# Kernel optimization log

Measured on AMD Instinct MI355X. Metric: run time of the kernel, lower is better.

## Reference

```python
import jax, jax.numpy as jnp
import numpy as np

D = 768
H = 12
W = 128
HD = D // H
EPS = 1e-5


def setup_inputs() -> dict:
    key = jax.random.key(0)
    ks = jax.random.split(key, 10)
    B, L = 4, 8190
    s = 1.0 / np.sqrt(D)
    inp = {
        "expanded": jax.random.normal(ks[0], (B, L, D), dtype=jnp.float32),
        "Wq": jax.random.normal(ks[1], (D, D), dtype=jnp.float32) * s,
        "bq": jnp.zeros((D,), jnp.float32),
        "Wk": jax.random.normal(ks[2], (D, D), dtype=jnp.float32) * s,
        "bk": jnp.zeros((D,), jnp.float32),
        "Wv": jax.random.normal(ks[3], (D, D), dtype=jnp.float32) * s,
        "bv": jnp.zeros((D,), jnp.float32),
        "Wo": jax.random.normal(ks[4], (D, D), dtype=jnp.float32) * s,
        "bo": jnp.zeros((D,), jnp.float32),
        "ln_g": jnp.ones((D,), jnp.float32),
        "ln_b": jnp.zeros((D,), jnp.float32),
    }
    return inp


def _local_attn(x, Wq, bq, Wk, bk, Wv, bv, Wo, bo):
    # x: (B, Lp, D) with Lp % W == 0; block-local multihead attention per window
    B, Lp, _ = x.shape
    nW = Lp // W
    xw = x.reshape(B, nW, W, D)
    q = (xw @ Wq + bq).reshape(B, nW, W, H, HD)
    k = (xw @ Wk + bk).reshape(B, nW, W, H, HD)
    v = (xw @ Wv + bv).reshape(B, nW, W, H, HD)
    scale = 1.0 / jnp.sqrt(jnp.asarray(HD, x.dtype))
    # scores: (B, nW, H, W, W)
    scores = jnp.einsum("bnqhd,bnkhd->bnhqk", q, k) * scale
    p = jax.nn.softmax(scores, axis=-1)
    o = jnp.einsum("bnhqk,bnkhd->bnqhd", p, v).reshape(B, nW, W, D)
    o = o @ Wo + bo
    return o.reshape(B, Lp, D)


def reference(expanded, Wq, bq, Wk, bk, Wv, bv, Wo, bo, ln_g, ln_b):
    B, L, _ = expanded.shape
    pad_len = (W - L % W) % W
    x = jnp.pad(expanded, ((0, 0), (0, pad_len), (0, 0))) if pad_len > 0 else expanded
    attn = _local_attn(x, Wq, bq, Wk, bk, Wv, bv, Wo, bo)
    attn = attn[:, :L, :]
    y = expanded + attn
    mu = jnp.mean(y, axis=-1, keepdims=True)
    var = jnp.mean(jnp.square(y - mu), axis=-1, keepdims=True)
    return (y - mu) * jax.lax.rsqrt(var + EPS) * ln_g + ln_b
```

## Files before the change

### kernel.cpp

```cpp
#include <hip/hip_runtime.h>
#include <hip/hip_bf16.h>

#define D 768
#define NQKV 2304
#define NH 12
#define HD 64
#define BATCH 4
#define LSEQ 8190
#define LPAD 8192
#define TP (BATCH*LPAD)

typedef __bf16 bf16x8 __attribute__((ext_vector_type(8)));
typedef float f32x4 __attribute__((ext_vector_type(4)));
using bf16 = __hip_bfloat16;

__device__ __forceinline__ float b2f(bf16 x){ return __bfloat162float(x); }
__device__ __forceinline__ bf16 f2b(float x){ return __float2bfloat16(x); }
__device__ __forceinline__ f32x4 mfma16(bf16x8 a, bf16x8 b, f32x4 c){
    return __builtin_amdgcn_mfma_f32_16x16x32_bf16(a, b, c, 0, 0, 0);
}
__device__ __forceinline__ void gload_lds16(const void* g, void* l){
    __builtin_amdgcn_global_load_lds(
        (const __attribute__((address_space(1))) unsigned int*)g,
        (__attribute__((address_space(3))) unsigned int*)l, 16, 0, 0);
}

__global__ void k_transpose(const float* __restrict__ w0, const float* __restrict__ w1,
                            const float* __restrict__ w2, const float* __restrict__ w3,
                            bf16* __restrict__ WqkvT, bf16* __restrict__ WoT) {
    const float* src; bf16* dst;
    switch (blockIdx.y) {
        case 0:  src = w0; dst = WqkvT;               break;
        case 1:  src = w1; dst = WqkvT + D * D;       break;
        case 2:  src = w2; dst = WqkvT + 2 * D * D;   break;
        default: src = w3; dst = WoT;                 break;
    }
    int o = blockIdx.x * 256 + threadIdx.x;
    int n = o / D, k = o % D;
    dst[o] = f2b(src[k * D + n]);
}

__global__ __launch_bounds__(256) void k_prep(const float* __restrict__ X,
                                              bf16* __restrict__ Xb, int tok0)
{
    int idx = (blockIdx.x * 256 + threadIdx.x) * 8;
    int row = idx / D, col = idx % D;
    int gt = tok0 + row, b = gt >> 13, pos = gt & 8191;
    bf16 tmp[8];
    if (pos < LSEQ) {
        const float* s = &X[((size_t)b * LSEQ + pos) * D + col];
        float4 f0 = *reinterpret_cast<const float4*>(s);
        float4 f1 = *reinterpret_cast<const float4*>(s + 4);
        tmp[0]=f2b(f0.x); tmp[1]=f2b(f0.y); tmp[2]=f2b(f0.z); tmp[3]=f2b(f0.w);
        tmp[4]=f2b(f1.x); tmp[5]=f2b(f1.y); tmp[6]=f2b(f1.z); tmp[7]=f2b(f1.w);
    } else {
        #pragma unroll
        for (int j = 0; j < 8; ++j) tmp[j] = f2b(0.f);
    }
    *reinterpret_cast<uint4*>(&Xb[idx]) = *reinterpret_cast<const uint4*>(tmp);
}

__global__ __launch_bounds__(512, 2) void k_gemm_qkv(
    const bf16* __restrict__ Xb, const bf16* __restrict__ Wt,
    const float* __restrict__ bq, const float* __restrict__ bk, const float* __restrict__ bv,
    bf16* __restrict__ Qkv)
{
    __shared__ alignas(16) bf16 a_lds[4 * 8192];
    __shared__ alignas(16) bf16 b_lds[4 * 8192];

    const int tid = threadIdx.x;
    const int wave = tid >> 6, lane = tid & 63, quad = lane >> 4, lm = lane & 15;
    const int wm = wave >> 2, wn = wave & 3;

    int bid = blockIdx.x;
    const int nwg = gridDim.x;
    if ((nwg & 7) == 0) { const int cpx = nwg >> 3; bid = (bid & 7) * cpx + (bid >> 3); }
    const int rt = bid / 9, ct = bid % 9;

    const int r_loc = tid >> 2;
    const int swslot = ((tid & 3) ^ ((r_loc >> 1) & 3)) * 8;
    const bf16* a_src = Xb + (size_t)(rt * 256 + r_loc) * D + swslot;
    const bf16* b_src = Wt + (size_t)(ct * 256 + r_loc) * D + swslot;
    const int dA = wave * 512;

    #pragma unroll
    for (int pt = 0; pt < 3; ++pt) {
        bf16* ab = a_lds + pt * 8192;
        bf16* bb = b_lds + pt * 8192;
        const int ko = pt * 32;
        gload_lds16(a_src + ko,           ab + dA);
        gload_lds16(a_src + 128 * D + ko, ab + 4096 + dA);
        gload_lds16(b_src + ko,           bb + dA);
        gload_lds16(b_src + 128 * D + ko, bb + 4096 + dA);
    }
    asm volatile("s_waitcnt vmcnt(8)" ::: "memory");
    __builtin_amdgcn_s_barrier();

    const int sw = (quad ^ ((lm >> 1) & 3)) * 8;
    const int aoff = (wm * 128 + lm) * 32 + sw;
    const int boff = (wn * 64 + lm) * 32 + sw;

    f32x4 acc[8][4] = {};

    #pragma unroll 1
    for (int t = 0; t < 24; ++t) {
        const bf16* ab = a_lds + (t & 3) * 8192;
        const bf16* bb = b_lds + (t & 3) * 8192;

        bf16x8 af[4], bfr[4];
        #pragma unroll
        for (int i = 0; i < 4; ++i)
            af[i] = *reinterpret_cast<const bf16x8*>(&ab[aoff + i * 512]);
        #pragma unroll
        for (int n = 0; n < 4; ++n)
            bfr[n] = *reinterpret_cast<const bf16x8*>(&bb[boff + n * 512]);
        if (t < 21) {
            bf16* abn = a_lds + ((t + 3) & 3) * 8192;
            const int ko = (t + 3) * 32;
            gload_lds16(a_src + ko,           abn + dA);
            gload_lds16(a_src + 128 * D + ko, abn + 4096 + dA);
        }
        __builtin_amdgcn_s_barrier();
        __builtin_amdgcn_s_setprio(1);
        #pragma unroll
        for (int i = 0; i < 4; ++i)
            #pragma unroll
            for (int n = 0; n < 4; ++n)
                acc[i][n] = mfma16(af[i], bfr[n], acc[i][n]);
        __builtin_amdgcn_s_setprio(0);
        __builtin_amdgcn_s_barrier();

        bf16x8 ag[4];
        #pragma unroll
        for (int i = 0; i < 4; ++i)
            ag[i] = *reinterpret_cast<const bf16x8*>(&ab[aoff + (i + 4) * 512]);
        if (t < 21) {
            bf16* bbn = b_lds + ((t + 3) & 3) * 8192;
            const int ko = (t + 3) * 32;
            gload_lds16(b_src + ko,           bbn + dA);
            gload_lds16(b_src + 128 * D + ko, bbn + 4096 + dA);
        }
        __builtin_amdgcn_s_barrier();
        __builtin_amdgcn_s_setprio(1);
        #pragma unroll
        for (int i = 0; i < 4; ++i)
            #pragma unroll
            for (int n = 0; n < 4; ++n)
                acc[i + 4][n] = mfma16(ag[i], bfr[n], acc[i + 4][n]);
        __builtin_amdgcn_s_setprio(0);

        if (t <= 20)      asm volatile("s_waitcnt vmcnt(8)" ::: "memory");
        else if (t == 21) asm volatile("s_waitcnt vmcnt(4)" ::: "memory");
        else if (t == 22) asm volatile("s_waitcnt vmcnt(0)" ::: "memory");
        if (t < 23) __builtin_amdgcn_s_barrier();
    }

    const float* bias; int cb;
    if (ct < 3)      { bias = bq; cb = ct * 256; }
    else if (ct < 6) { bias = bk; cb = ct * 256 - D; }
    else             { bias = bv; cb = ct * 256 - 2 * D; }
    float bvv[4];
    #pragma unroll
    for (int n = 0; n < 4; ++n)
        bvv[n] = bias[cb + wn * 64 + n * 16 + lm];

    const int row0 = rt * 256 + wm * 128 + quad * 4;
    const int col0 = ct * 256 + wn * 64 + lm;
    #pragma unroll
    for (int i = 0; i < 8; ++i)
        #pragma unroll
        for (int reg = 0; reg < 4; ++reg) {
            size_t r = (size_t)(row0 + i * 16 + reg) * NQKV;
            #pragma unroll
            for (int n = 0; n < 4; ++n)
                Qkv[r + col0 + n * 16] = f2b(acc[i][n][reg] + bvv[n]);
        }
}

__global__ __launch_bounds__(256) void k_oproj(
    const bf16* __restrict__ Aq, const bf16* __restrict__ WoT,
    const float* __restrict__ bo, const float* __restrict__ X,
    float* __restrict__ out, int tok0)
{
    __shared__ bf16 a_lds[128 * 32];
    __shared__ bf16 b_lds[128 * 32];
    const int tid = threadIdx.x;
    const int rt = blockIdx.x, ct = blockIdx.y;
    const int wave = tid >> 6, lane = tid & 63, quad = lane >> 4, lm = lane & 15;
    const int wm = wave >> 1, wn = wave & 1;
    const int seg0 = wave * 2, seg1 = seg0 + 1;
    const int srow = lane >> 2, selem = (lane & 3) * 8;

    const bf16* Ag = Aq + (size_t)(rt * 128) * NQKV;
    const bf16* Bg = WoT + (size_t)(ct * 128) * D;

    f32x4 acc[4][4] = {};

    for (int kt = 0; kt < D; kt += 32) {
        gload_lds16(Ag + (size_t)(seg0 * 16 + srow) * NQKV + kt + selem, &a_lds[seg0 * 512]);
        gload_lds16(Ag + (size_t)(seg1 * 16 + srow) * NQKV + kt + selem, &a_lds[seg1 * 512]);
        gload_lds16(Bg + (size_t)(seg0 * 16 + srow) * D + kt + selem, &b_lds[seg0 * 512]);
        gload_lds16(Bg + (size_t)(seg1 * 16 + srow) * D + kt + selem, &b_lds[seg1 * 512]);
        __syncthreads();
        bf16x8 af[4], bfr[4];
        #pragma unroll
        for (int i = 0; i < 4; ++i)
            af[i] = *reinterpret_cast<const bf16x8*>(&a_lds[(wm * 64 + i * 16 + lm) * 32 + quad * 8]);
        #pragma unroll
        for (int n = 0; n < 4; ++n)
            bfr[n] = *reinterpret_cast<const bf16x8*>(&b_lds[(wn * 64 + n * 16 + lm) * 32 + quad * 8]);
        #pragma unroll
        for (int i = 0; i < 4; ++i)
            #pragma unroll
            for (int n = 0; n < 4; ++n)
                acc[i][n] = mfma16(af[i], bfr[n], acc[i][n]);
        __syncthreads();
    }

    float bvv[4];
    #pragma unroll
    for (int n = 0; n < 4; ++n)
        bvv[n] = bo[ct * 128 + wn * 64 + n * 16 + lm];

    #pragma unroll
    for (int i = 0; i < 4; ++i)
        #pragma unroll
        for (int reg = 0; reg < 4; ++reg) {
            int g = tok0 + rt * 128 + wm * 64 + i * 16 + quad * 4 + reg;
            int b = g >> 13, pos = g & 8191;
            if (pos >= LSEQ) continue;
            size_t orow = (size_t)b * LSEQ + pos;
            #pragma unroll
            for (int n = 0; n < 4; ++n) {
                int col = ct * 128 + wn * 64 + n * 16 + lm;
                out[orow * D + col] = acc[i][n][reg] + bvv[n] + X[orow * D + col];
            }
        }
}

__global__ __launch_bounds__(256) void k_attn(bf16* Qkv)
{
    __shared__ bf16 qk_lds[2 * 128 * 72];
    __shared__ bf16 vt_lds[64 * 136];
    const int tid = threadIdx.x;
    const int g0 = blockIdx.x * 128, hc = blockIdx.y * 64;
    const int wave = tid >> 6, lane = tid & 63, quad = lane >> 4, lm = lane & 15;
    const int wq = wave * 32;
    bf16* Q_lds = qk_lds;
    bf16* K_lds = qk_lds + 128 * 72;
    bf16* P_lds = qk_lds;

    #pragma unroll
    for (int p = 0; p < 4; ++p) {
        int cid = tid + p * 256;
        int r = cid >> 3, cc = (cid & 7) * 8;
        size_t rb = (size_t)(g0 + r) * NQKV;
        *reinterpret_cast<uint4*>(&Q_lds[r * 72 + cc]) =
            *reinterpret_cast<const uint4*>(&Qkv[rb + hc + cc]);
        *reinterpret_cast<uint4*>(&K_lds[r * 72 + cc]) =
            *reinterpret_cast<const uint4*>(&Qkv[rb + D + hc + cc]);
        uint4 vv = *reinterpret_cast<const uint4*>(&Qkv[rb + 2 * D + hc + cc]);
        const bf16* ve = reinterpret_cast<const bf16*>(&vv);
        #pragma unroll
        for (int j = 0; j < 8; ++j) vt_lds[(cc + j) * 136 + r] = ve[j];
    }
    __syncthreads();

    f32x4 s[2][8] = {};
    #pragma unroll
    for (int ks = 0; ks < HD; ks += 32) {
        bf16x8 aq[2];
        #pragma unroll
        for (int i = 0; i < 2; ++i)
            aq[i] = *reinterpret_cast<const bf16x8*>(&Q_lds[(wq + i * 16 + lm) * 72 + ks + quad * 8]);
        #pragma unroll
        for (int nt = 0; nt < 8; ++nt) {
            bf16x8 bk = *reinterpret_cast<const bf16x8*>(&K_lds[(nt * 16 + lm) * 72 + ks + quad * 8]);
            s[0][nt] = mfma16(aq[0], bk, s[0][nt]);
            s[1][nt] = mfma16(aq[1], bk, s[1][nt]);
        }
    }
    __syncthreads();

    const float scale = 0.125f;
    #pragma unroll
    for (int i = 0; i < 2; ++i)
        #pragma unroll
        for (int reg = 0; reg < 4; ++reg) {
            float m = -1e30f;
            #pragma unroll
            for (int nt = 0; nt < 8; ++nt) m = fmaxf(m, s[i][nt][reg]);
            #pragma unroll
            for (int off = 8; off >= 1; off >>= 1) m = fmaxf(m, __shfl_xor(m, off));
            float pv[8]; float sum = 0.f;
            #pragma unroll
            for (int nt = 0; nt < 8; ++nt) {
                float p = __expf((s[i][nt][reg] - m) * scale);
                pv[nt] = p; sum += p;
            }
            #pragma unroll
            for (int off = 8; off >= 1; off >>= 1) sum += __shfl_xor(sum, off);
            float rinv = 1.f / sum;
            int row = wq + i * 16 + quad * 4 + reg;
            #pragma unroll
            for (int nt = 0; nt < 8; ++nt)
                P_lds[row * 136 + nt * 16 + lm] = f2b(pv[nt] * rinv);
        }
    __syncthreads();

    f32x4 o[2][4] = {};
    #pragma unroll
    for (int ks = 0; ks < 128; ks += 32) {
        bf16x8 ap[2];
        #pragma unroll
        for (int i = 0; i < 2; ++i)
            ap[i] = *reinterpret_cast<const bf16x8*>(&P_lds[(wq + i * 16 + lm) * 136 + ks + quad * 8]);
        #pragma unroll
        for (int n = 0; n < 4; ++n) {
            bf16x8 bv = *reinterpret_cast<const bf16x8*>(&vt_lds[(n * 16 + lm) * 136 + ks + quad * 8]);
            o[0][n] = mfma16(ap[0], bv, o[0][n]);
            o[1][n] = mfma16(ap[1], bv, o[1][n]);
        }
    }
    #pragma unroll
    for (int i = 0; i < 2; ++i)
        #pragma unroll
        for (int reg = 0; reg < 4; ++reg) {
            int row = wq + i * 16 + quad * 4 + reg;
            #pragma unroll
            for (int n = 0; n < 4; ++n)
                Qkv[(size_t)(g0 + row) * NQKV + hc + n * 16 + lm] = f2b(o[i][n][reg]);
        }
}

__global__ __launch_bounds__(256) void k_ln(const float* __restrict__ g_,
                                            const float* __restrict__ b_,
                                            float* __restrict__ y)
{
    __shared__ float red[256];
    const size_t base = (size_t)blockIdx.x * D;
    const int tid = threadIdx.x;
    float v[3];
    #pragma unroll
    for (int j = 0; j < 3; ++j) v[j] = y[base + tid + j * 256];

    red[tid] = v[0] + v[1] + v[2];
    __syncthreads();
    for (int o = 128; o > 0; o >>= 1) {
        if (tid < o) red[tid] += red[tid + o];
        __syncthreads();
    }
    float mu = red[0] * (1.f / 768.f);
    __syncthreads();

    float d0 = v[0] - mu, d1 = v[1] - mu, d2 = v[2] - mu;
    red[tid] = d0 * d0 + d1 * d1 + d2 * d2;
    __syncthreads();
    for (int o = 128; o > 0; o >>= 1) {
        if (tid < o) red[tid] += red[tid + o];
        __syncthreads();
    }
    float var = red[0] * (1.f / 768.f);
    float r = rsqrtf(var + 1e-5f);

    #pragma unroll
    for (int j = 0; j < 3; ++j) {
        int c = tid + j * 256;
        y[base + c] = (v[j] - mu) * r * g_[c] + b_[c];
    }
}

extern "C" void kernel_launch(void* const* d_in, const int* in_sizes, int n_in,
                              void* d_out, int out_size, void* d_ws, size_t ws_size,
                              hipStream_t stream)
{
    const float* expanded = (const float*)d_in[0];
    const float* Wq = (const float*)d_in[1];
    const float* bq = (const float*)d_in[2];
    const float* Wk = (const float*)d_in[3];
    const float* bk = (const float*)d_in[4];
    const float* Wv = (const float*)d_in[5];
    const float* bv = (const float*)d_in[6];
    const float* Wo = (const float*)d_in[7];
    const float* bo = (const float*)d_in[8];
    const float* ln_g = (const float*)d_in[9];
    const float* ln_b = (const float*)d_in[10];
    float* out = (float*)d_out;

    char* ws = (char*)d_ws;
    const size_t WSZ = (size_t)D * D * sizeof(bf16);
    bf16* WqkvT = (bf16*)(ws);
    bf16* WoT   = (bf16*)(ws + 3 * WSZ);
    const size_t fixed = 4 * WSZ;

    int cht = TP;
    while (cht > 256 && fixed + (size_t)cht * (D + NQKV) * sizeof(bf16) > ws_size)
        cht >>= 1;
    bf16* Xb  = (bf16*)(ws + fixed);
    bf16* Qkv = (bf16*)(ws + fixed + (size_t)cht * D * sizeof(bf16));

    k_transpose<<<dim3((D * D) / 256, 4), 256, 0, stream>>>(Wq, Wk, Wv, Wo, WqkvT, WoT);

    for (int t0 = 0; t0 < TP; t0 += cht) {
        k_prep<<<(cht * D) / 2048, 256, 0, stream>>>(expanded, Xb, t0);
        k_gemm_qkv<<<dim3((cht / 256) * 9), 512, 0, stream>>>(
            Xb, WqkvT, bq, bk, bv, Qkv);
        k_attn<<<dim3(cht / 128, NH), 256, 0, stream>>>(Qkv);
        k_oproj<<<dim3(cht / 128, D / 128), 256, 0, stream>>>(
            Qkv, WoT, bo, expanded, out, t0);
    }

    k_ln<<<BATCH * LSEQ, 256, 0, stream>>>(ln_g, ln_b, out);
}
```

Baseline: 523.9 us.

## Fuse output projection with residual LayerNorm and retile QKV GEMM pipeline

```diff
diff --git a/kernel.cpp b/kernel.cpp
--- a/kernel.cpp
+++ b/kernel.cpp
@@ -23,6 +23,12 @@
     __builtin_amdgcn_global_load_lds(
         (const __attribute__((address_space(1))) unsigned int*)g,
         (__attribute__((address_space(3))) unsigned int*)l, 16, 0, 0);
+}
+template<int N> __device__ __forceinline__ void vwait(){
+    asm volatile("s_waitcnt vmcnt(%0)" :: "n"(N) : "memory");
+}
+__device__ __forceinline__ void lgkm0(){
+    asm volatile("s_waitcnt lgkmcnt(0)" ::: "memory");
 }
 
 __global__ void k_transpose(const float* __restrict__ w0, const float* __restrict__ w1,
@@ -65,8 +71,8 @@
     const float* __restrict__ bq, const float* __restrict__ bk, const float* __restrict__ bv,
     bf16* __restrict__ Qkv)
 {
-    __shared__ alignas(16) bf16 a_lds[4 * 8192];
-    __shared__ alignas(16) bf16 b_lds[4 * 8192];
+    __shared__ alignas(16) bf16 a_lds[2 * 256 * 64];
+    __shared__ alignas(16) bf16 b_lds[2 * 256 * 64];
 
     const int tid = threadIdx.x;
     const int wave = tid >> 6, lane = tid & 63, quad = lane >> 4, lm = lane & 15;
@@ -77,82 +83,79 @@
     if ((nwg & 7) == 0) { const int cpx = nwg >> 3; bid = (bid & 7) * cpx + (bid >> 3); }
     const int rt = bid / 9, ct = bid % 9;
 
-    const int r_loc = tid >> 2;
-    const int swslot = ((tid & 3) ^ ((r_loc >> 1) & 3)) * 8;
-    const bf16* a_src = Xb + (size_t)(rt * 256 + r_loc) * D + swslot;
-    const bf16* b_src = Wt + (size_t)(ct * 256 + r_loc) * D + swslot;
-    const int dA = wave * 512;
-
-    #pragma unroll
-    for (int pt = 0; pt < 3; ++pt) {
-        bf16* ab = a_lds + pt * 8192;
-        bf16* bb = b_lds + pt * 8192;
-        const int ko = pt * 32;
-        gload_lds16(a_src + ko,           ab + dA);
-        gload_lds16(a_src + 128 * D + ko, ab + 4096 + dA);
-        gload_lds16(b_src + ko,           bb + dA);
-        gload_lds16(b_src + 128 * D + ko, bb + 4096 + dA);
-    }
-    asm volatile("s_waitcnt vmcnt(8)" ::: "memory");
+    const int srow = tid >> 3;
+    const int ssl  = ((tid & 7) ^ (srow & 7)) * 8;
+    const bf16* a_src = Xb + (size_t)(rt * 256 + srow) * D + ssl;
+    const bf16* b_src = Wt + (size_t)(ct * 256 + srow) * D + ssl;
+    const int ldsW = wave * 512;
+
+    auto stageA = [&](int T, int h) {
+        bf16* d = a_lds + (T & 1) * 16384 + h * 8192 + ldsW;
+        const bf16* s = a_src + (size_t)(h * 128) * D + T * 64;
+        gload_lds16(s, d);
+        gload_lds16(s + (size_t)64 * D, d + 4096);
+    };
+    auto stageB = [&](int T, int h) {
+        bf16* d = b_lds + (T & 1) * 16384 + h * 8192 + ldsW;
+        const bf16* s = b_src + (size_t)(h * 128) * D + T * 64;
+        gload_lds16(s, d);
+        gload_lds16(s + (size_t)64 * D, d + 4096);
+    };
+
+    const int swf0 = ((0 + quad) ^ (lm & 7)) * 8;
+    const int swf1 = ((4 + quad) ^ (lm & 7)) * 8;
+    const int arow0 = wm * 32 + lm;
+    const int brow0 = wn * 64 + lm;
+
+    f32x4 acc[8][4] = {};
+
+    stageB(0, 0); stageB(0, 1); stageA(0, 0); stageA(0, 1);
+    vwait<2>();
     __builtin_amdgcn_s_barrier();
 
-    const int sw = (quad ^ ((lm >> 1) & 3)) * 8;
-    const int aoff = (wm * 128 + lm) * 32 + sw;
-    const int boff = (wn * 64 + lm) * 32 + sw;
-
-    f32x4 acc[8][4] = {};
-
-    #pragma unroll 1
-    for (int t = 0; t < 24; ++t) {
-        const bf16* ab = a_lds + (t & 3) * 8192;
-        const bf16* bb = b_lds + (t & 3) * 8192;
-
-        bf16x8 af[4], bfr[4];
-        #pragma unroll
-        for (int i = 0; i < 4; ++i)
-            af[i] = *reinterpret_cast<const bf16x8*>(&ab[aoff + i * 512]);
-        #pragma unroll
-        for (int n = 0; n < 4; ++n)
-            bfr[n] = *reinterpret_cast<const bf16x8*>(&bb[boff + n * 512]);
-        if (t < 21) {
-            bf16* abn = a_lds + ((t + 3) & 3) * 8192;
-            const int ko = (t + 3) * 32;
-            gload_lds16(a_src + ko,           abn + dA);
-            gload_lds16(a_src + 128 * D + ko, abn + 4096 + dA);
-        }
-        __builtin_amdgcn_s_barrier();
-        __builtin_amdgcn_s_setprio(1);
-        #pragma unroll
-        for (int i = 0; i < 4; ++i)
-            #pragma unroll
-            for (int n = 0; n < 4; ++n)
-                acc[i][n] = mfma16(af[i], bfr[n], acc[i][n]);
-        __builtin_amdgcn_s_setprio(0);
-        __builtin_amdgcn_s_barrier();
-
-        bf16x8 ag[4];
-        #pragma unroll
-        for (int i = 0; i < 4; ++i)
-            ag[i] = *reinterpret_cast<const bf16x8*>(&ab[aoff + (i + 4) * 512]);
-        if (t < 21) {
-            bf16* bbn = b_lds + ((t + 3) & 3) * 8192;
-            const int ko = (t + 3) * 32;
-            gload_lds16(b_src + ko,           bbn + dA);
-            gload_lds16(b_src + 128 * D + ko, bbn + 4096 + dA);
-        }
-        __builtin_amdgcn_s_barrier();
-        __builtin_amdgcn_s_setprio(1);
-        #pragma unroll
-        for (int i = 0; i < 4; ++i)
-            #pragma unroll
-            for (int n = 0; n < 4; ++n)
-                acc[i + 4][n] = mfma16(ag[i], bfr[n], acc[i + 4][n]);
-        __builtin_amdgcn_s_setprio(0);
-
-        if (t <= 20)      asm volatile("s_waitcnt vmcnt(8)" ::: "memory");
-        else if (t == 21) asm volatile("s_waitcnt vmcnt(4)" ::: "memory");
-        else if (t == 22) asm volatile("s_waitcnt vmcnt(0)" ::: "memory");
-        if (t < 23) __builtin_amdgcn_s_barrier();
+    #pragma unroll
+    for (int t = 0; t < 12; ++t) {
+        const bf16* ab = a_lds + (t & 1) * 16384;
+        const bf16* bb = b_lds + (t & 1) * 16384;
+        bf16x8 bfr[4][2];
+        #pragma unroll
+        for (int p = 0; p < 4; ++p) {
+            bf16x8 af[2][2];
+            #pragma unroll
+            for (int i = 0; i < 2; ++i) {
+                const int r = (p * 64 + arow0 + i * 16) * 64;
+                af[i][0] = *reinterpret_cast<const bf16x8*>(&ab[r + swf0]);
+                af[i][1] = *reinterpret_cast<const bf16x8*>(&ab[r + swf1]);
+            }
+            if (p == 0) {
+                #pragma unroll
+                for (int n = 0; n < 4; ++n) {
+                    const int r = (brow0 + n * 16) * 64;
+                    bfr[n][0] = *reinterpret_cast<const bf16x8*>(&bb[r + swf0]);
+                    bfr[n][1] = *reinterpret_cast<const bf16x8*>(&bb[r + swf1]);
+                }
+            }
+            if (t < 11) {
+                if (p == 0) stageB(t + 1, 0);
+                if (p == 1) stageB(t + 1, 1);
+                if (p == 2) stageA(t + 1, 0);
+                if (p == 3) stageA(t + 1, 1);
+            }
+            __builtin_amdgcn_s_barrier();
+            lgkm0();
+            __builtin_amdgcn_s_setprio(1);
+            #pragma unroll
+            for (int ks = 0; ks < 2; ++ks)
+                #pragma unroll
+                for (int i = 0; i < 2; ++i)
+                    #pragma unroll
+                    for (int n = 0; n < 4; ++n)
+                        acc[p * 2 + i][n] = mfma16(af[i][ks], bfr[n][ks], acc[p * 2 + i][n]);
+            __builtin_amdgcn_s_setprio(0);
+            if (p == 1) { if (t < 11) vwait<4>(); else vwait<0>(); }
+            if (p == 3 && t < 11) vwait<2>();
+            if (!(p == 3 && t == 11)) __builtin_amdgcn_s_barrier();
+        }
     }
 
     const float* bias; int cb;
@@ -164,77 +167,16 @@
     for (int n = 0; n < 4; ++n)
         bvv[n] = bias[cb + wn * 64 + n * 16 + lm];
 
-    const int row0 = rt * 256 + wm * 128 + quad * 4;
     const int col0 = ct * 256 + wn * 64 + lm;
     #pragma unroll
-    for (int i = 0; i < 8; ++i)
+    for (int j = 0; j < 8; ++j)
         #pragma unroll
         for (int reg = 0; reg < 4; ++reg) {
-            size_t r = (size_t)(row0 + i * 16 + reg) * NQKV;
+            int row = rt * 256 + (j >> 1) * 64 + wm * 32 + (j & 1) * 16 + quad * 4 + reg;
+            size_t rb = (size_t)row * NQKV;
             #pragma unroll
             for (int n = 0; n < 4; ++n)
-                Qkv[r + col0 + n * 16] = f2b(acc[i][n][reg] + bvv[n]);
-        }
-}
-
-__global__ __launch_bounds__(256) void k_oproj(
-    const bf16* __restrict__ Aq, const bf16* __restrict__ WoT,
-    const float* __restrict__ bo, const float* __restrict__ X,
-    float* __restrict__ out, int tok0)
-{
-    __shared__ bf16 a_lds[128 * 32];
-    __shared__ bf16 b_lds[128 * 32];
-    const int tid = threadIdx.x;
-    const int rt = blockIdx.x, ct = blockIdx.y;
-    const int wave = tid >> 6, lane = tid & 63, quad = lane >> 4, lm = lane & 15;
-    const int wm = wave >> 1, wn = wave & 1;
-    const int seg0 = wave * 2, seg1 = seg0 + 1;
-    const int srow = lane >> 2, selem = (lane & 3) * 8;
-
-    const bf16* Ag = Aq + (size_t)(rt * 128) * NQKV;
-    const bf16* Bg = WoT + (size_t)(ct * 128) * D;
-
-    f32x4 acc[4][4] = {};
-
-    for (int kt = 0; kt < D; kt += 32) {
-        gload_lds16(Ag + (size_t)(seg0 * 16 + srow) * NQKV + kt + selem, &a_lds[seg0 * 512]);
-        gload_lds16(Ag + (size_t)(seg1 * 16 + srow) * NQKV + kt + selem, &a_lds[seg1 * 512]);
-        gload_lds16(Bg + (size_t)(seg0 * 16 + srow) * D + kt + selem, &b_lds[seg0 * 512]);
-        gload_lds16(Bg + (size_t)(seg1 * 16 + srow) * D + kt + selem, &b_lds[seg1 * 512]);
-        __syncthreads();
-        bf16x8 af[4], bfr[4];
-        #pragma unroll
-        for (int i = 0; i < 4; ++i)
-            af[i] = *reinterpret_cast<const bf16x8*>(&a_lds[(wm * 64 + i * 16 + lm) * 32 + quad * 8]);
-        #pragma unroll
-        for (int n = 0; n < 4; ++n)
-            bfr[n] = *reinterpret_cast<const bf16x8*>(&b_lds[(wn * 64 + n * 16 + lm) * 32 + quad * 8]);
-        #pragma unroll
-        for (int i = 0; i < 4; ++i)
-            #pragma unroll
-            for (int n = 0; n < 4; ++n)
-                acc[i][n] = mfma16(af[i], bfr[n], acc[i][n]);
-        __syncthreads();
-    }
-
-    float bvv[4];
-    #pragma unroll
-    for (int n = 0; n < 4; ++n)
-        bvv[n] = bo[ct * 128 + wn * 64 + n * 16 + lm];
-
-    #pragma unroll
-    for (int i = 0; i < 4; ++i)
-        #pragma unroll
-        for (int reg = 0; reg < 4; ++reg) {
-            int g = tok0 + rt * 128 + wm * 64 + i * 16 + quad * 4 + reg;
-            int b = g >> 13, pos = g & 8191;
-            if (pos >= LSEQ) continue;
-            size_t orow = (size_t)b * LSEQ + pos;
-            #pragma unroll
-            for (int n = 0; n < 4; ++n) {
-                int col = ct * 128 + wn * 64 + n * 16 + lm;
-                out[orow * D + col] = acc[i][n][reg] + bvv[n] + X[orow * D + col];
-            }
+                Qkv[rb + col0 + n * 16] = f2b(acc[j][n][reg] + bvv[n]);
         }
 }
 
@@ -333,41 +275,142 @@
         }
 }
 
-__global__ __launch_bounds__(256) void k_ln(const float* __restrict__ g_,
-                                            const float* __restrict__ b_,
-                                            float* __restrict__ y)
+__global__ __launch_bounds__(1024, 4) void k_oproj_ln(
+    const bf16* __restrict__ Aq, const bf16* __restrict__ WoT,
+    const float* __restrict__ bo, const float* __restrict__ X,
+    const float* __restrict__ ln_g, const float* __restrict__ ln_b,
+    float* __restrict__ out, int tok0)
 {
-    __shared__ float red[256];
-    const size_t base = (size_t)blockIdx.x * D;
+    __shared__ alignas(16) bf16 a_lds[2 * 128 * 64];
+    __shared__ alignas(16) bf16 b_lds[2 * 768 * 32];
+    __shared__ float red[128][18];
+
     const int tid = threadIdx.x;
-    float v[3];
-    #pragma unroll
-    for (int j = 0; j < 3; ++j) v[j] = y[base + tid + j * 256];
-
-    red[tid] = v[0] + v[1] + v[2];
+    const int wave = tid >> 6, lane = tid & 63, quad = lane >> 4, lm = lane & 15;
+    const int wm = wave >> 3, wn = wave & 7;
+    const int blk128 = blockIdx.x * 128;
+
+    const int asl = ((tid & 7) ^ ((tid >> 3) & 7)) * 8;
+    const int bsl = ((tid & 3) ^ ((tid >> 2) & 3)) * 8;
+    const bf16* a_srcp = Aq + (size_t)(blk128 + (tid >> 3)) * NQKV + asl;
+
+    auto stageAo = [&](int P) {
+        bf16* d = a_lds + (P & 1) * 8192 + wave * 512;
+        gload_lds16(a_srcp + P * 64, d);
+    };
+    auto stageBo = [&](int T, int c) {
+        bf16* d = b_lds + (T & 1) * 24576 + c * 8192 + wave * 512;
+        const bf16* s = WoT + (size_t)(c * 256 + (tid >> 2)) * D + T * 32 + bsl;
+        gload_lds16(s, d);
+    };
+
+    const int swA0 = ((0 + quad) ^ (lm & 7)) * 8;
+    const int swA1 = ((4 + quad) ^ (lm & 7)) * 8;
+    const int swB  = (quad ^ (lm & 3)) * 8;
+    const int arow = wm * 64 + lm;
+    const int brow = wn * 96 + lm;
+
+    f32x4 acc[4][6] = {};
+
+    stageBo(0, 0); stageBo(0, 1); stageBo(0, 2); stageAo(0);
+    vwait<0>();
+    __builtin_amdgcn_s_barrier();
+
+    #pragma unroll
+    for (int t = 0; t < 24; ++t) {
+        const bf16* ab = a_lds + ((t >> 1) & 1) * 8192;
+        const bf16* bb = b_lds + (t & 1) * 24576;
+        const int swA = (t & 1) ? swA1 : swA0;
+        bf16x8 af[4], bf0[3];
+        #pragma unroll
+        for (int i = 0; i < 4; ++i)
+            af[i] = *reinterpret_cast<const bf16x8*>(&ab[(arow + i * 16) * 64 + swA]);
+        #pragma unroll
+        for (int n = 0; n < 3; ++n)
+            bf0[n] = *reinterpret_cast<const bf16x8*>(&bb[(brow + n * 16) * 32 + swB]);
+        if (t + 1 < 24) { stageBo(t + 1, 0); stageBo(t + 1, 1); stageBo(t + 1, 2); }
+        if ((t & 1) == 0 && (t >> 1) + 1 < 12) stageAo((t >> 1) + 1);
+        __builtin_amdgcn_s_barrier();
+        lgkm0();
+        __builtin_amdgcn_s_setprio(1);
+        #pragma unroll
+        for (int i = 0; i < 4; ++i)
+            #pragma unroll
+            for (int n = 0; n < 3; ++n)
+                acc[i][n] = mfma16(af[i], bf0[n], acc[i][n]);
+        bf16x8 bf1[3];
+        #pragma unroll
+        for (int n = 0; n < 3; ++n)
+            bf1[n] = *reinterpret_cast<const bf16x8*>(&bb[(brow + (n + 3) * 16) * 32 + swB]);
+        #pragma unroll
+        for (int i = 0; i < 4; ++i)
+            #pragma unroll
+            for (int n = 0; n < 3; ++n)
+                acc[i][n + 3] = mfma16(af[i], bf1[n], acc[i][n + 3]);
+        __builtin_amdgcn_s_setprio(0);
+        if (t < 23) {
+            if ((t & 1) == 0 && t < 22) vwait<1>(); else vwait<0>();
+            __builtin_amdgcn_s_barrier();
+        }
+    }
+
+    float bov[6], gv[6], bbv[6];
+    #pragma unroll
+    for (int n = 0; n < 6; ++n) {
+        int c = wn * 96 + n * 16 + lm;
+        bov[n] = bo[c]; gv[n] = ln_g[c]; bbv[n] = ln_b[c];
+    }
+
+    #pragma unroll
+    for (int i = 0; i < 4; ++i)
+        #pragma unroll
+        for (int reg = 0; reg < 4; ++reg) {
+            int r = wm * 64 + i * 16 + quad * 4 + reg;
+            int gt = tok0 + blk128 + r, b = gt >> 13, pos = gt & 8191;
+            bool live = pos < LSEQ;
+            size_t xrow = ((size_t)b * LSEQ + pos) * D;
+            float s = 0.f, sq = 0.f;
+            #pragma unroll
+            for (int n = 0; n < 6; ++n) {
+                int c = wn * 96 + n * 16 + lm;
+                float y = acc[i][n][reg] + bov[n] + (live ? X[xrow + c] : 0.f);
+                acc[i][n][reg] = y;
+                s += y; sq += y * y;
+            }
+            #pragma unroll
+            for (int off = 1; off <= 8; off <<= 1) {
+                s  += __shfl_xor(s, off);
+                sq += __shfl_xor(sq, off);
+            }
+            if (lm == 0) { red[r][wn] = s; red[r][8 + wn] = sq; }
+        }
     __syncthreads();
-    for (int o = 128; o > 0; o >>= 1) {
-        if (tid < o) red[tid] += red[tid + o];
-        __syncthreads();
-    }
-    float mu = red[0] * (1.f / 768.f);
+    if (tid < 128) {
+        float s = 0.f, sq = 0.f;
+        #pragma unroll
+        for (int w = 0; w < 8; ++w) { s += red[tid][w]; sq += red[tid][8 + w]; }
+        float mu = s * (1.f / 768.f);
+        float var = sq * (1.f / 768.f) - mu * mu;
+        red[tid][16] = mu;
+        red[tid][17] = rsqrtf(var + 1e-5f);
+    }
     __syncthreads();
 
-    float d0 = v[0] - mu, d1 = v[1] - mu, d2 = v[2] - mu;
-    red[tid] = d0 * d0 + d1 * d1 + d2 * d2;
-    __syncthreads();
-    for (int o = 128; o > 0; o >>= 1) {
-        if (tid < o) red[tid] += red[tid + o];
-        __syncthreads();
-    }
-    float var = red[0] * (1.f / 768.f);
-    float r = rsqrtf(var + 1e-5f);
-
-    #pragma unroll
-    for (int j = 0; j < 3; ++j) {
-        int c = tid + j * 256;
-        y[base + c] = (v[j] - mu) * r * g_[c] + b_[c];
-    }
+    #pragma unroll
+    for (int i = 0; i < 4; ++i)
+        #pragma unroll
+        for (int reg = 0; reg < 4; ++reg) {
+            int r = wm * 64 + i * 16 + quad * 4 + reg;
+            int gt = tok0 + blk128 + r, b = gt >> 13, pos = gt & 8191;
+            if (pos >= LSEQ) continue;
+            size_t orow = ((size_t)b * LSEQ + pos) * D;
+            float mu = red[r][16], rs = red[r][17];
+            #pragma unroll
+            for (int n = 0; n < 6; ++n) {
+                int c = wn * 96 + n * 16 + lm;
+                out[orow + c] = (acc[i][n][reg] - mu) * rs * gv[n] + bbv[n];
+            }
+        }
 }
 
 extern "C" void kernel_launch(void* const* d_in, const int* in_sizes, int n_in,
@@ -406,9 +449,7 @@
         k_gemm_qkv<<<dim3((cht / 256) * 9), 512, 0, stream>>>(
             Xb, WqkvT, bq, bk, bv, Qkv);
         k_attn<<<dim3(cht / 128, NH), 256, 0, stream>>>(Qkv);
-        k_oproj<<<dim3(cht / 128, D / 128), 256, 0, stream>>>(
-            Qkv, WoT, bo, expanded, out, t0);
-    }
-
-    k_ln<<<BATCH * LSEQ, 256, 0, stream>>>(ln_g, ln_b, out);
-}
+        k_oproj_ln<<<dim3(cht / 128), 1024, 0, stream>>>(
+            Qkv, WoT, bo, expanded, ln_g, ln_b, out, t0);
+    }
+}
```

Measured after the change: 609.0 us. 16.2% more time.
